# Kernel tuning notes

Measured on AMD Instinct MI355X. Metric: run time of the kernel, lower is better.

## Reference

```python
import jax, jax.numpy as jnp
import numpy as np

OUT_SIZE = 7
SAMPLE_RATIO = 2
NUM_ROI = 128


def setup_inputs() -> dict:
    key = jax.random.key(0)
    k1, k2, k3 = jax.random.split(key, 3)
    B, H, W, C = 8, 32, 32, 256
    feature_maps = jax.random.normal(k1, (B, H, W, C), dtype=jnp.float32)
    # boxes in pixel coords [x1, y1, x2, y2], guaranteed x1 < x2, y1 < y2
    lo = jax.random.uniform(k2, (B, NUM_ROI, 2), dtype=jnp.float32) * 16.0
    sz = 4.0 + jax.random.uniform(k3, (B, NUM_ROI, 2), dtype=jnp.float32) * 11.0
    hi = jnp.minimum(lo + sz, 31.0)
    boxes = jnp.concatenate([lo, hi], axis=-1)  # [B, R, 4]
    return {"feature_maps": feature_maps, "boxes": boxes}


def _roi_align(feature_maps, boxes):
    B, H, W, C = feature_maps.shape
    R = boxes.shape[1]
    S = OUT_SIZE * SAMPLE_RATIO  # crop size per side
    N = B * R

    # normalize boxes by (input_size - 1), as in the module
    scale = jnp.array([W - 1.0, H - 1.0, W - 1.0, H - 1.0], dtype=feature_maps.dtype)
    b = boxes.reshape(N, 4) / scale
    x1 = jnp.maximum(b[:, 0], 0.0)
    y1 = jnp.maximum(b[:, 1], 0.0)
    x2 = jnp.minimum(b[:, 2], 1.0)
    y2 = jnp.minimum(b[:, 3], 1.0)

    bin_h = (y2 - y1) / OUT_SIZE
    bin_w = (x2 - x1) / OUT_SIZE
    gy1 = y1 + 0.5 * bin_h / SAMPLE_RATIO
    gx1 = x1 + 0.5 * bin_w / SAMPLE_RATIO
    gy2 = y2 - 0.5 * bin_h / SAMPLE_RATIO
    gx2 = x2 - 0.5 * bin_w / SAMPLE_RATIO

    # tf.image.crop_and_resize sample coordinates (crop size S > 1):
    # in_y = y1*(H-1) + i*(y2-y1)*(H-1)/(S-1)
    i = jnp.arange(S, dtype=feature_maps.dtype)
    ys = gy1[:, None] * (H - 1) + i[None, :] * ((gy2 - gy1) * (H - 1) / (S - 1))[:, None]  # [N,S]
    xs = gx1[:, None] * (W - 1) + i[None, :] * ((gx2 - gx1) * (W - 1) / (S - 1))[:, None]  # [N,S]

    y0 = jnp.floor(ys)
    x0 = jnp.floor(xs)
    wy = (ys - y0)[:, :, None, None]  # [N,S,1,1]
    wx = (xs - x0)[:, None, :, None]  # [N,1,S,1]

    y0i = jnp.clip(y0.astype(jnp.int32), 0, H - 1)
    y1i = jnp.clip(y0.astype(jnp.int32) + 1, 0, H - 1)
    x0i = jnp.clip(x0.astype(jnp.int32), 0, W - 1)
    x1i = jnp.clip(x0.astype(jnp.int32) + 1, 0, W - 1)

    b_idx = jnp.repeat(jnp.arange(B, dtype=jnp.int32), R)[:, None, None]  # [N,1,1]
    yr0 = y0i[:, :, None]  # [N,S,1]
    yr1 = y1i[:, :, None]
    xr0 = x0i[:, None, :]  # [N,1,S]
    xr1 = x1i[:, None, :]

    v00 = feature_maps[b_idx, yr0, xr0]  # [N,S,S,C]
    v01 = feature_maps[b_idx, yr0, xr1]
    v10 = feature_maps[b_idx, yr1, xr0]
    v11 = feature_maps[b_idx, yr1, xr1]

    top = v00 + (v01 - v00) * wx
    bot = v10 + (v11 - v10) * wx
    sampled = top + (bot - top) * wy  # [N,S,S,C]

    # avg_pool2d with kernel = stride = SAMPLE_RATIO
    pooled = sampled.reshape(N, OUT_SIZE, SAMPLE_RATIO, OUT_SIZE, SAMPLE_RATIO, C).mean(axis=(2, 4))
    return pooled.reshape(B, R, OUT_SIZE, OUT_SIZE, C)


def reference(feature_maps, boxes):
    return _roi_align(feature_maps, boxes)
```

## Files before the change

### kernel.cpp

```cpp
#include <hip/hip_runtime.h>


#define NB 8
#define NH 32
#define NW 32
#define NR 128

__device__ __forceinline__ float4 lerp4(float4 a, float4 b, float w) {
    float4 r;
    r.x = a.x + (b.x - a.x) * w;
    r.y = a.y + (b.y - a.y) * w;
    r.z = a.z + (b.z - a.z) * w;
    r.w = a.w + (b.w - a.w) * w;
    return r;
}

template<int DY>
__device__ __forceinline__ void roi_row_proc(
    const float4* __restrict__ basep,
    int ro0, int ro1, int ro2, int ro3,
    int xlo, float basex, float stepx,
    float wy0, float wy1,
    float4* __restrict__ outp)
{
    auto vsum_col = [&](int cidx) -> float4 {
        int xo = (min(cidx, NW - 1)) << 6;
        float4 r0 = basep[ro0 + xo];
        float4 r1 = basep[ro1 + xo];
        float4 lo = lerp4(r0, r1, wy0);
        float4 hi;
        if constexpr (DY == 0) {
            hi = lerp4(r0, r1, wy1);
        } else if constexpr (DY == 1) {
            float4 r2 = basep[ro2 + xo];
            hi = lerp4(r1, r2, wy1);
        } else {
            float4 r2 = basep[ro2 + xo];
            float4 r3 = basep[ro3 + xo];
            hi = lerp4(r2, r3, wy1);
        }
        float4 v;
        v.x = lo.x + hi.x; v.y = lo.y + hi.y;
        v.z = lo.z + hi.z; v.w = lo.w + hi.w;
        return v;
    };

    float4 va = vsum_col(xlo);
    int s = 0;
    float xsf = basex;
    float gf = floorf(xsf);
    int gn = __builtin_amdgcn_readfirstlane((int)gf) - xlo;
    float wx = xsf - gf;
    float4 acc = make_float4(0.f, 0.f, 0.f, 0.f);

    #pragma unroll
    for (int ci = 0; ci < 15; ++ci) {
        float4 vb = vsum_col(xlo + ci + 1);
        while (s < 14 && gn == ci) {
            float4 p = lerp4(va, vb, wx);
            if ((s & 1) == 0) {
                acc = p;
            } else {
                float4 r;
                r.x = (acc.x + p.x) * 0.25f;
                r.y = (acc.y + p.y) * 0.25f;
                r.z = (acc.z + p.z) * 0.25f;
                r.w = (acc.w + p.w) * 0.25f;
                outp[(s >> 1) << 6] = r;
            }
            ++s;
            xsf = basex + (float)s * stepx;
            gf = floorf(xsf);
            gn = __builtin_amdgcn_readfirstlane((int)gf) - xlo;
            wx = xsf - gf;
        }
        va = vb;
    }
}

__global__ __launch_bounds__(256) void roi_align_colmajor(
    const float* __restrict__ fm,
    const float* __restrict__ boxes,
    float* __restrict__ out)
{
    int bid = blockIdx.x;
    int newbid = (bid & 7) * 224 + (bid >> 3);
    int t = threadIdx.x;
    int lane = t & 63;
    int g = newbid * 4 + (t >> 6);
    int n = (int)(((unsigned)g * 9363u) >> 16);
    int oy = g - n * 7;
    int b = n >> 7;

    float bx0 = boxes[n * 4 + 0] * (1.0f / 31.0f);
    float by0 = boxes[n * 4 + 1] * (1.0f / 31.0f);
    float bx1 = boxes[n * 4 + 2] * (1.0f / 31.0f);
    float by1 = boxes[n * 4 + 3] * (1.0f / 31.0f);
    float x1 = fmaxf(bx0, 0.0f), y1 = fmaxf(by0, 0.0f);
    float x2 = fminf(bx1, 1.0f), y2 = fminf(by1, 1.0f);
    float bin_h = (y2 - y1) / 7.0f;
    float bin_w = (x2 - x1) / 7.0f;
    float gy1 = y1 + 0.25f * bin_h;
    float gx1 = x1 + 0.25f * bin_w;
    float gy2 = y2 - 0.25f * bin_h;
    float gx2 = x2 - 0.25f * bin_w;
    float basey = gy1 * 31.0f;
    float basex = gx1 * 31.0f;
    float stepy = (gy2 - gy1) * (31.0f / 13.0f);
    float stepx = (gx2 - gx1) * (31.0f / 13.0f);

    float ysf0 = basey + (float)(2 * oy) * stepy;
    float ysf1 = basey + (float)(2 * oy + 1) * stepy;
    float f0f = floorf(ysf0);
    float f1f = floorf(ysf1);
    float wy0 = ysf0 - f0f;
    float wy1 = ysf1 - f1f;
    int f0 = (int)f0f;
    int dy = __builtin_amdgcn_readfirstlane((int)f1f - f0);

    const float4* fm4 = (const float4*)fm;
    const float4* basep = fm4 + (size_t)b * (NH * NW * 64) + lane;
    int ro0 = (min(f0,     NH - 1) * NW) << 6;
    int ro1 = (min(f0 + 1, NH - 1) * NW) << 6;
    int ro2 = (min(f0 + 2, NH - 1) * NW) << 6;
    int ro3 = (min(f0 + 3, NH - 1) * NW) << 6;

    int xlo = __builtin_amdgcn_readfirstlane((int)floorf(basex));
    float4* outp = (float4*)out + (n * 49 + oy * 7) * 64 + lane;

    if (dy == 0)      roi_row_proc<0>(basep, ro0, ro1, ro2, ro3, xlo, basex, stepx, wy0, wy1, outp);
    else if (dy == 1) roi_row_proc<1>(basep, ro0, ro1, ro2, ro3, xlo, basex, stepx, wy0, wy1, outp);
    else              roi_row_proc<2>(basep, ro0, ro1, ro2, ro3, xlo, basex, stepx, wy0, wy1, outp);
}

extern "C" void kernel_launch(void* const* d_in, const int* in_sizes, int n_in,
                              void* d_out, int out_size, void* d_ws, size_t ws_size,
                              hipStream_t stream) {
    const float* fm    = (const float*)d_in[0];
    const float* boxes = (const float*)d_in[1];
    float* out = (float*)d_out;

    roi_align_colmajor<<<1792, 256, 0, stream>>>(fm, boxes, out);
}
```

Measured before the change: 21.84 us.

## Prefetch feature columns through a 4-slot register ring and precount samples per column

New measurement: 22.42 us. +2.6%, slower.

```diff
diff --git a/kernel.cpp b/kernel.cpp
--- a/kernel.cpp
+++ b/kernel.cpp
@@ -23,42 +23,56 @@
     float wy0, float wy1,
     float4* __restrict__ outp)
 {
-    auto vsum_col = [&](int cidx) -> float4 {
-        int xo = (min(cidx, NW - 1)) << 6;
-        float4 r0 = basep[ro0 + xo];
-        float4 r1 = basep[ro1 + xo];
-        float4 lo = lerp4(r0, r1, wy0);
+    float4 ring[4][4];
+
+#define LOADSLOT(S, cidx) do {                                   \
+        int xo_ = (min((cidx), NW - 1)) << 6;                    \
+        ring[S][0] = basep[ro0 + xo_];                           \
+        ring[S][1] = basep[ro1 + xo_];                           \
+        if constexpr (DY >= 1) ring[S][2] = basep[ro2 + xo_];    \
+        if constexpr (DY == 2) ring[S][3] = basep[ro3 + xo_];    \
+    } while (0)
+
+    LOADSLOT(0, xlo);
+    LOADSLOT(1, xlo + 1);
+    LOADSLOT(2, xlo + 2);
+    LOADSLOT(3, xlo + 3);
+
+    unsigned long long cnt3 = 0;
+    #pragma unroll
+    for (int s2 = 0; s2 < 14; ++s2) {
+        float xsf = fmaf((float)s2, stepx, basex);
+        int gi = __builtin_amdgcn_readfirstlane((int)floorf(xsf));
+        cnt3 += 1ull << (3 * (gi - xlo));
+    }
+
+    auto VSUM = [&](int S) -> float4 {
+        float4 lo = lerp4(ring[S][0], ring[S][1], wy0);
         float4 hi;
-        if constexpr (DY == 0) {
-            hi = lerp4(r0, r1, wy1);
-        } else if constexpr (DY == 1) {
-            float4 r2 = basep[ro2 + xo];
-            hi = lerp4(r1, r2, wy1);
-        } else {
-            float4 r2 = basep[ro2 + xo];
-            float4 r3 = basep[ro3 + xo];
-            hi = lerp4(r2, r3, wy1);
-        }
+        if constexpr (DY == 0)      hi = lerp4(ring[S][0], ring[S][1], wy1);
+        else if constexpr (DY == 1) hi = lerp4(ring[S][1], ring[S][2], wy1);
+        else                        hi = lerp4(ring[S][2], ring[S][3], wy1);
         float4 v;
         v.x = lo.x + hi.x; v.y = lo.y + hi.y;
         v.z = lo.z + hi.z; v.w = lo.w + hi.w;
         return v;
     };
 
-    float4 va = vsum_col(xlo);
-    int s = 0;
-    float xsf = basex;
-    float gf = floorf(xsf);
-    int gn = __builtin_amdgcn_readfirstlane((int)gf) - xlo;
-    float wx = xsf - gf;
+    float4 va = VSUM(0);
+    float sf = 0.0f;
+    int srun = 0;
     float4 acc = make_float4(0.f, 0.f, 0.f, 0.f);
 
     #pragma unroll
     for (int ci = 0; ci < 15; ++ci) {
-        float4 vb = vsum_col(xlo + ci + 1);
-        while (s < 14 && gn == ci) {
+        float4 vb = VSUM((ci + 1) & 3);
+        if (ci <= 11) LOADSLOT(ci & 3, xlo + ci + 4);
+        int c = (int)((cnt3 >> (3 * ci)) & 7);
+        for (int k = 0; k < c; ++k) {
+            float xsf = fmaf(sf, stepx, basex);
+            float wx = xsf - (float)(xlo + ci);
             float4 p = lerp4(va, vb, wx);
-            if ((s & 1) == 0) {
+            if ((srun & 1) == 0) {
                 acc = p;
             } else {
                 float4 r;
@@ -66,19 +80,17 @@
                 r.y = (acc.y + p.y) * 0.25f;
                 r.z = (acc.z + p.z) * 0.25f;
                 r.w = (acc.w + p.w) * 0.25f;
-                outp[(s >> 1) << 6] = r;
+                outp[(srun >> 1) << 6] = r;
             }
-            ++s;
-            xsf = basex + (float)s * stepx;
-            gf = floorf(xsf);
-            gn = __builtin_amdgcn_readfirstlane((int)gf) - xlo;
-            wx = xsf - gf;
+            ++srun;
+            sf += 1.0f;
         }
         va = vb;
     }
+#undef LOADSLOT
 }
 
-__global__ __launch_bounds__(256) void roi_align_colmajor(
+__global__ __launch_bounds__(256) void roi_align_pipe(
     const float* __restrict__ fm,
     const float* __restrict__ boxes,
     float* __restrict__ out)
@@ -140,5 +152,5 @@
     const float* boxes = (const float*)d_in[1];
     float* out = (float*)d_out;
 
-    roi_align_colmajor<<<1792, 256, 0, stream>>>(fm, boxes, out);
+    roi_align_pipe<<<1792, 256, 0, stream>>>(fm, boxes, out);
 }
```
